# Performance work log

Measured on AMD Instinct MI355X. Metric: run time of the kernel, lower is better.

## Reference

```python
import jax, jax.numpy as jnp
import numpy as np

N = 100000
E = 1600000
IN_DIM, HID, OUT = 128, 64, 32
SLOPE = 0.1


def setup_inputs() -> dict:
    key = jax.random.key(0)
    ks = jax.random.split(key, 8)
    x = jax.random.normal(ks[0], (N, IN_DIM), dtype=jnp.float32)
    edge_index = jax.random.randint(ks[1], (2, E), 0, N, dtype=jnp.int64)
    s1 = 1.0 / np.sqrt(IN_DIM)
    s2 = 1.0 / np.sqrt(HID)
    W_l1 = jax.random.uniform(ks[2], (IN_DIM, HID), jnp.float32, -s1, s1)
    W_r1 = jax.random.uniform(ks[3], (IN_DIM, HID), jnp.float32, -s1, s1)
    b1 = jax.random.uniform(ks[4], (HID,), jnp.float32, -s1, s1)
    W_l2 = jax.random.uniform(ks[5], (HID, OUT), jnp.float32, -s2, s2)
    W_r2 = jax.random.uniform(ks[6], (HID, OUT), jnp.float32, -s2, s2)
    b2 = jax.random.uniform(ks[7], (OUT,), jnp.float32, -s2, s2)
    return {"x": x, "edge_index": edge_index,
            "W_l1": W_l1, "W_r1": W_r1, "b1": b1,
            "W_l2": W_l2, "W_r2": W_r2, "b2": b2}


def _sage_conv(h, src, dst, deg_inv, W_l, W_r, b):
    # mean-aggregate neighbor features: gather from src, scatter-add to dst
    agg = jax.ops.segment_sum(h[src], dst, num_segments=N) * deg_inv  # [N, d]
    return agg @ W_l + h @ W_r + b


def reference(x, edge_index, W_l1, W_r1, b1, W_l2, W_r2, b2):
    src, dst = edge_index[0], edge_index[1]
    deg = jax.ops.segment_sum(jnp.ones((E,), x.dtype), dst, num_segments=N)
    deg_inv = (1.0 / jnp.maximum(deg, 1.0))[:, None]  # [N, 1]
    h = jax.nn.leaky_relu(_sage_conv(x, src, dst, deg_inv, W_l1, W_r1, b1), SLOPE)
    z = jax.nn.leaky_relu(_sage_conv(h, src, dst, deg_inv, W_l2, W_r2, b2), SLOPE)
    return z
```

## Files before the change

### kernel.cpp

```cpp
#include <hip/hip_runtime.h>


constexpr int IN_DIM  = 128;
constexpr int HID     = 64;
constexpr int OUT_DIM = 32;
constexpr float SLOPE = 0.1f;
constexpr int NPB_SHIFT = 8;
constexpr int NBMAX = 512;
constexpr int CHUNK = 4096;
constexpr int SUBCAP = 4096;

typedef unsigned int uint32;
typedef unsigned short ushort16;
typedef unsigned char uchar8;
using floatx2 = __attribute__((ext_vector_type(2))) float;

__device__ inline float blo(uint32 u) { return __uint_as_float(u << 16); }
__device__ inline float bhi(uint32 u) { return __uint_as_float(u & 0xffff0000u); }
__device__ inline ushort16 f2b(float f) {
    uint32 u = __float_as_uint(f);
    u += 0x7fffu + ((u >> 16) & 1u);
    return (ushort16)(u >> 16);
}
__device__ inline uint32 pack2(float lo, float hi) {
    return (uint32)f2b(lo) | ((uint32)f2b(hi) << 16);
}
__device__ inline float lrelu(float v) { return (v > 0.f) ? v : SLOPE * v; }
__device__ inline void addup(float* acc, uint4 u) {
    acc[0] += blo(u.x); acc[1] += bhi(u.x);
    acc[2] += blo(u.y); acc[3] += bhi(u.y);
    acc[4] += blo(u.z); acc[5] += bhi(u.z);
    acc[6] += blo(u.w); acc[7] += bhi(u.w);
}
__device__ inline uchar8 f2fp8(float f) {
    uint32 r = (uint32)__builtin_amdgcn_cvt_pk_fp8_f32(f, f, 0, false);
    return (uchar8)(r & 0xffu);
}
__device__ inline void addp4(float* acc, uint32 w) {
    floatx2 a = __builtin_amdgcn_cvt_pk_f32_fp8((int)w, false);
    floatx2 b = __builtin_amdgcn_cvt_pk_f32_fp8((int)w, true);
    acc[0] += a[0]; acc[1] += a[1]; acc[2] += b[0]; acc[3] += b[1];
}
__device__ inline void addq8(float* acc, uint2 u) {
    addp4(acc + 0, u.x); addp4(acc + 4, u.y);
}

__global__ __launch_bounds__(256) void prep_kernel(
    const float* __restrict__ Wl1, const float* __restrict__ Wr1,
    const float* __restrict__ Wl2, const float* __restrict__ Wr2,
    ushort16* __restrict__ Wb1, ushort16* __restrict__ Wb2,
    int* __restrict__ bhist, int* __restrict__ done) {
    const int gid = blockIdx.x * 256 + threadIdx.x;
    if (gid < NBMAX) bhist[gid] = 0;
    if (gid == NBMAX) *done = 0;
    for (int i = gid; i < 128 * 128; i += gridDim.x * 256) {
        int c = i >> 7, k = i & 127;
        Wb1[i] = f2b((c < HID) ? Wl1[k * HID + c] : Wr1[k * HID + (c - HID)]);
    }
    for (int i = gid; i < 64 * 64; i += gridDim.x * 256) {
        int c = i >> 6, k = i & 63;
        Wb2[i] = f2b((c < OUT_DIM) ? Wl2[k * OUT_DIM + c]
                                   : Wr2[k * OUT_DIM + (c - OUT_DIM)]);
    }
}

__global__ __launch_bounds__(256) void hist_scan_kernel(
    const int* __restrict__ dst, int* __restrict__ bhist,
    int* __restrict__ pbase, int* __restrict__ bcur,
    int* __restrict__ done, int E, int NB) {
    __shared__ int bh[NBMAX];
    __shared__ int s2[256];
    __shared__ int flag;
    const int tid = threadIdx.x;
    for (int i = tid; i < NBMAX; i += 256) bh[i] = 0;
    __syncthreads();
    for (int e = blockIdx.x * 256 + tid; e < E; e += gridDim.x * 256)
        atomicAdd(&bh[dst[e] >> NPB_SHIFT], 1);
    __syncthreads();
    for (int b = tid; b < NBMAX; b += 256)
        if (bh[b]) atomicAdd(&bhist[b], bh[b]);
    __threadfence();
    if (tid == 0) flag = (atomicAdd(done, 1) == (int)gridDim.x - 1) ? 1 : 0;
    __syncthreads();
    if (!flag) return;
    __threadfence();
    int v0 = atomicAdd(&bhist[2 * tid], 0);
    int v1 = atomicAdd(&bhist[2 * tid + 1], 0);
    int p0 = (v0 + 15) & ~15, p1 = (v1 + 15) & ~15;
    s2[tid] = p0 + p1; __syncthreads();
    for (int off = 1; off < 256; off <<= 1) {
        int b = (tid >= off) ? s2[tid - off] : 0;
        __syncthreads();
        s2[tid] += b;
        __syncthreads();
    }
    int base = s2[tid] - (p0 + p1);
    pbase[2 * tid]     = base;      bcur[2 * tid]     = base;
    pbase[2 * tid + 1] = base + p0; bcur[2 * tid + 1] = base + p0;
}

__global__ __launch_bounds__(256) void gemm1_part_kernel(
    const float* __restrict__ x, const ushort16* __restrict__ Wb1,
    const float* __restrict__ b1,
    const int* __restrict__ src, const int* __restrict__ dst,
    int* __restrict__ bcur, uint32* __restrict__ pairs,
    ushort16* __restrict__ xl, float* __restrict__ xr,
    int N, int E, int NB, int npart) {
    using frag = __attribute__((ext_vector_type(8))) short;
    using f32x4 = __attribute__((ext_vector_type(4))) float;
    constexpr int LDA = IN_DIM + 8;
    __shared__ union {
        struct {
            int hist[NBMAX], loff[NBMAX], cur[NBMAX], gbase[NBMAX];
            int s[256];
            uint32 stage[CHUNK];
        } p;
        ushort16 Ash[64][LDA];
    } sm;
    const int tid = threadIdx.x;
    if (blockIdx.x < npart) {
        const int e0  = blockIdx.x * CHUNK;
        const int cnt = min(CHUNK, E - e0);
        for (int i = tid; i < NBMAX; i += 256) sm.p.hist[i] = 0;
        __syncthreads();
        int sreg[16], dreg[16];
#pragma unroll
        for (int k = 0; k < 16; ++k) {
            int i = tid + k * 256;
            if (i < cnt) {
                sreg[k] = src[e0 + i];
                dreg[k] = dst[e0 + i];
                atomicAdd(&sm.p.hist[dreg[k] >> NPB_SHIFT], 1);
            }
        }
        __syncthreads();
        int a0 = sm.p.hist[2 * tid], a1 = sm.p.hist[2 * tid + 1];
        sm.p.s[tid] = a0 + a1; __syncthreads();
        for (int off = 1; off < 256; off <<= 1) {
            int t = (tid >= off) ? sm.p.s[tid - off] : 0;
            __syncthreads();
            sm.p.s[tid] += t;
            __syncthreads();
        }
        int ex = sm.p.s[tid] - (a0 + a1);
        sm.p.loff[2 * tid] = ex;      sm.p.loff[2 * tid + 1] = ex + a0;
        sm.p.cur[2 * tid]  = ex;      sm.p.cur[2 * tid + 1]  = ex + a0;
        __syncthreads();
#pragma unroll
        for (int k = 0; k < 16; ++k) {
            int i = tid + k * 256;
            if (i < cnt) {
                int b = dreg[k] >> NPB_SHIFT;
                int pos = atomicAdd(&sm.p.cur[b], 1);
                sm.p.stage[pos] = (uint32)sreg[k] | ((uint32)(dreg[k] & 255) << 24);
            }
        }
        __syncthreads();
        for (int b = tid; b < NB; b += 256) {
            int cb = sm.p.hist[b];
            if (cb) sm.p.gbase[b] = atomicAdd(&bcur[b], cb);
        }
        __syncthreads();
        for (int i = tid; i < cnt; i += 256) {
            int lo = 0, hi = NB - 1;
            while (lo < hi) {
                int mid = (lo + hi + 1) >> 1;
                if (sm.p.loff[mid] <= i) lo = mid; else hi = mid - 1;
            }
            pairs[sm.p.gbase[lo] + (i - sm.p.loff[lo])] = sm.p.stage[i];
        }
        return;
    }
    const int n0 = (blockIdx.x - npart) * 64;
    {
        const int lc = (tid & 31) * 4;
        for (int row = tid >> 5; row < 64; row += 8) {
            int node = n0 + row;
            float4 xv = (node < N)
                ? *reinterpret_cast<const float4*>(&x[(long)node * IN_DIM + lc])
                : float4{0.f, 0.f, 0.f, 0.f};
            ushort16 pk[4] = {f2b(xv.x), f2b(xv.y), f2b(xv.z), f2b(xv.w)};
            *reinterpret_cast<ushort2*>(&sm.Ash[row][lc])     = ushort2{pk[0], pk[1]};
            *reinterpret_cast<ushort2*>(&sm.Ash[row][lc + 2]) = ushort2{pk[2], pk[3]};
        }
    }
    __syncthreads();
    const int lane = tid & 63;
    const int m0   = (tid >> 6) * 16;
    const int mlo  = lane & 15;
    const int qk   = lane >> 4;
    frag Af[4];
#pragma unroll
    for (int kc = 0; kc < 4; ++kc)
        Af[kc] = *reinterpret_cast<const frag*>(&sm.Ash[m0 + mlo][kc * 32 + qk * 8]);
#pragma unroll
    for (int ct = 0; ct < 8; ++ct) {
        f32x4 acc = {0.f, 0.f, 0.f, 0.f};
#pragma unroll
        for (int kc = 0; kc < 4; ++kc) {
            frag Bf = *reinterpret_cast<const frag*>(
                &Wb1[(ct * 16 + mlo) * 128 + kc * 32 + qk * 8]);
            acc = __builtin_amdgcn_mfma_f32_16x16x32_bf16(Af[kc], Bf, acc, 0, 0, 0);
        }
        const int col = ct * 16 + mlo;
#pragma unroll
        for (int r = 0; r < 4; ++r) {
            int node = n0 + m0 + qk * 4 + r;
            if (node < N) {
                if (col < HID) xl[(long)node * HID + col] = f2b(acc[r]);
                else           xr[(long)node * HID + (col - HID)] = acc[r] + b1[col - HID];
            }
        }
    }
}

__global__ __launch_bounds__(512) void agg1_gemm2_kernel(
    const uint32* __restrict__ pairs, const int* __restrict__ bhist,
    const int* __restrict__ pbase,
    const uint4* __restrict__ xlq, const float* __restrict__ xr,
    const ushort16* __restrict__ Wb2, const float* __restrict__ b2,
    uint32* __restrict__ srcs, int* __restrict__ rowptr, int* __restrict__ degA,
    uchar8* __restrict__ hl8, float* __restrict__ hr, int N) {
    using frag = __attribute__((ext_vector_type(8))) short;
    using f32x4 = __attribute__((ext_vector_type(4))) float;
    constexpr int LDH = HID + 8;
    __shared__ int hist[256], loff[256], cur[128];
    __shared__ int lsrc[SUBCAP];
    __shared__ ushort16 hsh[128][LDH];
    const int tid  = threadIdx.x;
    const int bkt  = blockIdx.x >> 1;
    const int half = blockIdx.x & 1;
    const int n0   = bkt << NPB_SHIFT;
    const int base = pbase[bkt];
    const int sz   = bhist[bkt];
    if (tid < 256) hist[tid] = 0;
    __syncthreads();
    for (int i = tid; i < sz; i += 512)
        atomicAdd(&hist[pairs[base + i] >> 24], 1);
    __syncthreads();
    int v = (tid < 256) ? hist[tid] : 0;
    if (tid < 256) loff[tid] = v;
    __syncthreads();
    for (int off = 1; off < 256; off <<= 1) {
        int t = (tid >= off && tid < 256) ? loff[tid - off] : 0;
        __syncthreads();
        if (tid < 256) loff[tid] += t;
        __syncthreads();
    }
    if (tid < 256) loff[tid] -= v;
    __syncthreads();
    if (half == 0 && tid < 256 && n0 + tid < N) {
        rowptr[n0 + tid] = base + loff[tid];
        degA[n0 + tid]   = hist[tid];
    }
    const int hbase = loff[half << 7];
    const int hcnt  = (half ? sz : loff[128]) - hbase;
    if (tid < 128) cur[tid] = loff[(half << 7) + tid] - hbase;
    __syncthreads();
    for (int i = tid; i < sz; i += 512) {
        uint32 u = pairs[base + i];
        int dl = u >> 24;
        if ((dl >> 7) == half) {
            int pos = atomicAdd(&cur[dl & 127], 1);
            lsrc[pos] = (int)(u & 0xFFFFFFu);
        }
    }
    __syncthreads();
    for (int i = tid; i < hcnt; i += 512)
        srcs[base + hbase + i] = (uint32)lsrc[i];
    const int lane = tid & 63;
    const int wid  = tid >> 6;
    const int li   = lane & 7;
#pragma unroll
    for (int pass = 0; pass < 2; ++pass) {
        const int nll = pass * 64 + wid * 8 + (lane >> 3);
        const int nl  = (half << 7) + nll;
        const int n   = n0 + nl;
        if (n >= N) continue;
        const int lo0 = loff[nl] - hbase;
        const int d   = hist[nl];
        float acc[8] = {};
        int j = 0;
        while (j + 16 <= d) {
            int i0[8], i1[8];
#pragma unroll
            for (int t = 0; t < 8; ++t) i0[t] = lsrc[lo0 + j + t];
#pragma unroll
            for (int t = 0; t < 8; ++t) i1[t] = lsrc[lo0 + j + 8 + t];
            uint4 u0[8], u1[8];
#pragma unroll
            for (int t = 0; t < 8; ++t) u0[t] = xlq[(long)i0[t] * 8 + li];
#pragma unroll
            for (int t = 0; t < 8; ++t) u1[t] = xlq[(long)i1[t] * 8 + li];
#pragma unroll
            for (int t = 0; t < 8; ++t) { addup(acc, u0[t]); addup(acc, u1[t]); }
            j += 16;
        }
        if (j + 8 <= d) {
            int i0[8];
#pragma unroll
            for (int t = 0; t < 8; ++t) i0[t] = lsrc[lo0 + j + t];
            uint4 u0[8];
#pragma unroll
            for (int t = 0; t < 8; ++t) u0[t] = xlq[(long)i0[t] * 8 + li];
#pragma unroll
            for (int t = 0; t < 8; ++t) addup(acc, u0[t]);
            j += 8;
        }
        for (; j < d; ++j) {
            uint4 u = xlq[(long)lsrc[lo0 + j] * 8 + li];
            addup(acc, u);
        }
        const float dinv = (d > 0) ? (1.f / (float)d) : 1.f;
        float4 xrA = *reinterpret_cast<const float4*>(&xr[(long)n * HID + 8 * li]);
        float4 xrB = *reinterpret_cast<const float4*>(&xr[(long)n * HID + 8 * li + 4]);
        float h[8];
        h[0] = fmaf(acc[0], dinv, xrA.x); h[1] = fmaf(acc[1], dinv, xrA.y);
        h[2] = fmaf(acc[2], dinv, xrA.z); h[3] = fmaf(acc[3], dinv, xrA.w);
        h[4] = fmaf(acc[4], dinv, xrB.x); h[5] = fmaf(acc[5], dinv, xrB.y);
        h[6] = fmaf(acc[6], dinv, xrB.z); h[7] = fmaf(acc[7], dinv, xrB.w);
#pragma unroll
        for (int t = 0; t < 8; ++t) h[t] = lrelu(h[t]);
        uint4 pk;
        pk.x = pack2(h[0], h[1]); pk.y = pack2(h[2], h[3]);
        pk.z = pack2(h[4], h[5]); pk.w = pack2(h[6], h[7]);
        *reinterpret_cast<uint4*>(&hsh[nll][li * 8]) = pk;
    }
    __syncthreads();
    const int m0  = wid * 16;
    const int mlo = lane & 15;
    const int qk  = lane >> 4;
    frag Af[2];
#pragma unroll
    for (int kc = 0; kc < 2; ++kc)
        Af[kc] = *reinterpret_cast<const frag*>(&hsh[m0 + mlo][kc * 32 + qk * 8]);
#pragma unroll
    for (int ct = 0; ct < 4; ++ct) {
        f32x4 acc = {0.f, 0.f, 0.f, 0.f};
#pragma unroll
        for (int kc = 0; kc < 2; ++kc) {
            frag Bf = *reinterpret_cast<const frag*>(
                &Wb2[(ct * 16 + mlo) * 64 + kc * 32 + qk * 8]);
            acc = __builtin_amdgcn_mfma_f32_16x16x32_bf16(Af[kc], Bf, acc, 0, 0, 0);
        }
        const int col = ct * 16 + mlo;
#pragma unroll
        for (int r = 0; r < 4; ++r) {
            int node = n0 + (half << 7) + m0 + qk * 4 + r;
            if (node < N) {
                if (col < OUT_DIM) hl8[(long)node * OUT_DIM + col] = f2fp8(acc[r]);
                else hr[(long)node * OUT_DIM + (col - OUT_DIM)] = acc[r] + b2[col - OUT_DIM];
            }
        }
    }
}

__global__ __launch_bounds__(256) void agg2_final_kernel(
    const int* __restrict__ rowptr, const int* __restrict__ degA,
    const uint32* __restrict__ srcs,
    const uint2* __restrict__ hlq, const float* __restrict__ hr,
    float* __restrict__ z, int N) {
    const int lane  = threadIdx.x & 63;
    const int li    = lane & 3;
    const int gbase = lane & 60;
    const int wave  = (blockIdx.x << 2) + (threadIdx.x >> 6);
    const int n     = wave * 16 + (lane >> 2);
    if (n >= N) return;
    const int rp = rowptr[n];
    const int d  = degA[n];
    float acc[8] = {};
    int j = 0;
    while (j + 16 <= d) {
        int sA = (int)srcs[rp + j + li];
        int sB = (int)srcs[rp + j + 4 + li];
        int sC = (int)srcs[rp + j + 8 + li];
        int sD = (int)srcs[rp + j + 12 + li];
        uint2 u[16];
#pragma unroll
        for (int t = 0; t < 4; ++t) u[t]      = hlq[(long)__shfl(sA, gbase + t) * 4 + li];
#pragma unroll
        for (int t = 0; t < 4; ++t) u[4 + t]  = hlq[(long)__shfl(sB, gbase + t) * 4 + li];
#pragma unroll
        for (int t = 0; t < 4; ++t) u[8 + t]  = hlq[(long)__shfl(sC, gbase + t) * 4 + li];
#pragma unroll
        for (int t = 0; t < 4; ++t) u[12 + t] = hlq[(long)__shfl(sD, gbase + t) * 4 + li];
#pragma unroll
        for (int t = 0; t < 16; ++t) addq8(acc, u[t]);
        j += 16;
    }
    while (j + 4 <= d) {
        int sA = (int)srcs[rp + j + li];
        uint2 u[4];
#pragma unroll
        for (int t = 0; t < 4; ++t) u[t] = hlq[(long)__shfl(sA, gbase + t) * 4 + li];
#pragma unroll
        for (int t = 0; t < 4; ++t) addq8(acc, u[t]);
        j += 4;
    }
    int r = d - j;
    if (r > 0) {
        int sA = (int)srcs[rp + j + ((li < r) ? li : 0)];
#pragma unroll
        for (int t = 0; t < 3; ++t) {
            if (t < r) {
                uint2 u = hlq[(long)__shfl(sA, gbase + t) * 4 + li];
                addq8(acc, u);
            }
        }
    }
    const float dinv = (d > 0) ? (1.f / (float)d) : 1.f;
    float4 hA = *reinterpret_cast<const float4*>(&hr[(long)n * OUT_DIM + 8 * li]);
    float4 hB = *reinterpret_cast<const float4*>(&hr[(long)n * OUT_DIM + 8 * li + 4]);
    float4 vA, vB;
    vA.x = lrelu(fmaf(acc[0], dinv, hA.x)); vA.y = lrelu(fmaf(acc[1], dinv, hA.y));
    vA.z = lrelu(fmaf(acc[2], dinv, hA.z)); vA.w = lrelu(fmaf(acc[3], dinv, hA.w));
    vB.x = lrelu(fmaf(acc[4], dinv, hB.x)); vB.y = lrelu(fmaf(acc[5], dinv, hB.y));
    vB.z = lrelu(fmaf(acc[6], dinv, hB.z)); vB.w = lrelu(fmaf(acc[7], dinv, hB.w));
    *reinterpret_cast<float4*>(&z[(long)n * OUT_DIM + 8 * li]) = vA;
    *reinterpret_cast<float4*>(&z[(long)n * OUT_DIM + 8 * li + 4]) = vB;
}

extern "C" void kernel_launch(void* const* d_in, const int* in_sizes, int n_in,
                              void* d_out, int out_size, void* d_ws, size_t ws_size,
                              hipStream_t stream) {
    const float* x   = (const float*)d_in[0];
    const int*   ei  = (const int*)d_in[1];
    const float* Wl1 = (const float*)d_in[2];
    const float* Wr1 = (const float*)d_in[3];
    const float* b1  = (const float*)d_in[4];
    const float* Wl2 = (const float*)d_in[5];
    const float* Wr2 = (const float*)d_in[6];
    const float* b2  = (const float*)d_in[7];

    const int N = in_sizes[0] / IN_DIM;
    const int E = in_sizes[1] / 2;
    const int* src = ei;
    const int* dst = ei + E;
    const int NB = (N + 255) >> NPB_SHIFT;

    char* p = (char*)d_ws;
    int* bhist    = (int*)p;           p += sizeof(int) * NBMAX;
    int* done     = (int*)p;           p += sizeof(int) * 4;
    int* pbase    = (int*)p;           p += sizeof(int) * NBMAX;
    int* bcur     = (int*)p;           p += sizeof(int) * NBMAX;
    int* rowptr   = (int*)p;           p += sizeof(int) * (N + 4);
    int* degA     = (int*)p;           p += sizeof(int) * (N + 4);
    uint32* pairs = (uint32*)p;        p += sizeof(uint32) * ((size_t)E + 16 * NBMAX);
    uint32* srcs  = (uint32*)p;        p += sizeof(uint32) * ((size_t)E + 16 * NBMAX);
    ushort16* Wb1 = (ushort16*)p;      p += sizeof(ushort16) * 128 * 128;
    ushort16* Wb2 = (ushort16*)p;      p += sizeof(ushort16) * 64 * 64;
    ushort16* xl  = (ushort16*)p;      p += sizeof(ushort16) * (size_t)N * HID;
    float* xr     = (float*)p;         p += sizeof(float) * (size_t)N * HID;
    uchar8* hl8   = (uchar8*)p;        p += sizeof(uchar8) * ((size_t)N * OUT_DIM + 64);
    float* hr     = (float*)p;         p += sizeof(float) * (size_t)N * OUT_DIM;

    const int ngemm = (N + 63) / 64;
    const int npart = (E + CHUNK - 1) / CHUNK;
    prep_kernel<<<32, 256, 0, stream>>>(Wl1, Wr1, Wl2, Wr2, Wb1, Wb2, bhist, done);
    hist_scan_kernel<<<256, 256, 0, stream>>>(dst, bhist, pbase, bcur, done, E, NB);
    gemm1_part_kernel<<<npart + ngemm, 256, 0, stream>>>(
        x, Wb1, b1, src, dst, bcur, pairs, xl, xr, N, E, NB, npart);
    agg1_gemm2_kernel<<<NB * 2, 512, 0, stream>>>(pairs, bhist, pbase,
                                                  (const uint4*)xl, xr, Wb2, b2,
                                                  srcs, rowptr, degA, hl8, hr, N);
    agg2_final_kernel<<<(N + 63) / 64, 256, 0, stream>>>(rowptr, degA, srcs,
                                                         (const uint2*)hl8, hr,
                                                         (float*)d_out, N);
}
```

Measured before the change: 278.7 us.

## Store root-term intermediates in bf16 and stage GEMM outputs through LDS

```diff
diff --git a/kernel.cpp b/kernel.cpp
--- a/kernel.cpp
+++ b/kernel.cpp
@@ -104,7 +104,7 @@
     const float* __restrict__ b1,
     const int* __restrict__ src, const int* __restrict__ dst,
     int* __restrict__ bcur, uint32* __restrict__ pairs,
-    ushort16* __restrict__ xl, float* __restrict__ xr,
+    ushort16* __restrict__ xl, ushort16* __restrict__ xr,
     int N, int E, int NB, int npart) {
     using frag = __attribute__((ext_vector_type(8))) short;
     using f32x4 = __attribute__((ext_vector_type(4))) float;
@@ -116,6 +116,7 @@
             uint32 stage[CHUNK];
         } p;
         ushort16 Ash[64][LDA];
+        ushort16 xst[2][64][64];
     } sm;
     const int tid = threadIdx.x;
     if (blockIdx.x < npart) {
@@ -193,6 +194,7 @@
 #pragma unroll
     for (int kc = 0; kc < 4; ++kc)
         Af[kc] = *reinterpret_cast<const frag*>(&sm.Ash[m0 + mlo][kc * 32 + qk * 8]);
+    __syncthreads();
 #pragma unroll
     for (int ct = 0; ct < 8; ++ct) {
         f32x4 acc = {0.f, 0.f, 0.f, 0.f};
@@ -205,11 +207,20 @@
         const int col = ct * 16 + mlo;
 #pragma unroll
         for (int r = 0; r < 4; ++r) {
-            int node = n0 + m0 + qk * 4 + r;
-            if (node < N) {
-                if (col < HID) xl[(long)node * HID + col] = f2b(acc[r]);
-                else           xr[(long)node * HID + (col - HID)] = acc[r] + b1[col - HID];
-            }
+            int row = m0 + qk * 4 + r;
+            if (col < HID) sm.xst[0][row][col] = f2b(acc[r]);
+            else           sm.xst[1][row][col - HID] = f2b(acc[r] + b1[col - HID]);
+        }
+    }
+    __syncthreads();
+    for (int idx = tid; idx < 64 * 8; idx += 256) {
+        int row = idx >> 3, ch = idx & 7;
+        int node = n0 + row;
+        if (node < N) {
+            reinterpret_cast<uint4*>(xl)[(long)node * 8 + ch] =
+                reinterpret_cast<const uint4*>(&sm.xst[0][0][0])[idx];
+            reinterpret_cast<uint4*>(xr)[(long)node * 8 + ch] =
+                reinterpret_cast<const uint4*>(&sm.xst[1][0][0])[idx];
         }
     }
 }
@@ -217,10 +228,10 @@
 __global__ __launch_bounds__(512) void agg1_gemm2_kernel(
     const uint32* __restrict__ pairs, const int* __restrict__ bhist,
     const int* __restrict__ pbase,
-    const uint4* __restrict__ xlq, const float* __restrict__ xr,
+    const uint4* __restrict__ xlq, const uint4* __restrict__ xrq,
     const ushort16* __restrict__ Wb2, const float* __restrict__ b2,
     uint32* __restrict__ srcs, int* __restrict__ rowptr, int* __restrict__ degA,
-    uchar8* __restrict__ hl8, float* __restrict__ hr, int N) {
+    uchar8* __restrict__ hl8, ushort16* __restrict__ hr, int N) {
     using frag = __attribute__((ext_vector_type(8))) short;
     using f32x4 = __attribute__((ext_vector_type(4))) float;
     constexpr int LDH = HID + 8;
@@ -312,13 +323,12 @@
             addup(acc, u);
         }
         const float dinv = (d > 0) ? (1.f / (float)d) : 1.f;
-        float4 xrA = *reinterpret_cast<const float4*>(&xr[(long)n * HID + 8 * li]);
-        float4 xrB = *reinterpret_cast<const float4*>(&xr[(long)n * HID + 8 * li + 4]);
+        uint4 xv = xrq[(long)n * 8 + li];
         float h[8];
-        h[0] = fmaf(acc[0], dinv, xrA.x); h[1] = fmaf(acc[1], dinv, xrA.y);
-        h[2] = fmaf(acc[2], dinv, xrA.z); h[3] = fmaf(acc[3], dinv, xrA.w);
-        h[4] = fmaf(acc[4], dinv, xrB.x); h[5] = fmaf(acc[5], dinv, xrB.y);
-        h[6] = fmaf(acc[6], dinv, xrB.z); h[7] = fmaf(acc[7], dinv, xrB.w);
+        h[0] = fmaf(acc[0], dinv, blo(xv.x)); h[1] = fmaf(acc[1], dinv, bhi(xv.x));
+        h[2] = fmaf(acc[2], dinv, blo(xv.y)); h[3] = fmaf(acc[3], dinv, bhi(xv.y));
+        h[4] = fmaf(acc[4], dinv, blo(xv.z)); h[5] = fmaf(acc[5], dinv, bhi(xv.z));
+        h[6] = fmaf(acc[6], dinv, blo(xv.w)); h[7] = fmaf(acc[7], dinv, bhi(xv.w));
 #pragma unroll
         for (int t = 0; t < 8; ++t) h[t] = lrelu(h[t]);
         uint4 pk;
@@ -327,6 +337,8 @@
         *reinterpret_cast<uint4*>(&hsh[nll][li * 8]) = pk;
     }
     __syncthreads();
+    unsigned char* hl_st = reinterpret_cast<unsigned char*>(lsrc);
+    ushort16* hr_st = reinterpret_cast<ushort16*>(lsrc + 1024);
     const int m0  = wid * 16;
     const int mlo = lane & 15;
     const int qk  = lane >> 4;
@@ -346,19 +358,32 @@
         const int col = ct * 16 + mlo;
 #pragma unroll
         for (int r = 0; r < 4; ++r) {
-            int node = n0 + (half << 7) + m0 + qk * 4 + r;
-            if (node < N) {
-                if (col < OUT_DIM) hl8[(long)node * OUT_DIM + col] = f2fp8(acc[r]);
-                else hr[(long)node * OUT_DIM + (col - OUT_DIM)] = acc[r] + b2[col - OUT_DIM];
-            }
-        }
+            int row = m0 + qk * 4 + r;
+            if (col < OUT_DIM) hl_st[row * 32 + col] = f2fp8(acc[r]);
+            else hr_st[row * 32 + (col - OUT_DIM)] = f2b(acc[r] + b2[col - OUT_DIM]);
+        }
+    }
+    __syncthreads();
+    for (int idx = tid; idx < 128 * 2; idx += 512) {
+        int row = idx >> 1, ch = idx & 1;
+        int node = n0 + (half << 7) + row;
+        if (node < N)
+            reinterpret_cast<uint4*>(hl8)[(long)node * 2 + ch] =
+                reinterpret_cast<const uint4*>(hl_st)[idx];
+    }
+    for (int idx = tid; idx < 128 * 4; idx += 512) {
+        int row = idx >> 2, ch = idx & 3;
+        int node = n0 + (half << 7) + row;
+        if (node < N)
+            reinterpret_cast<uint4*>(hr)[(long)node * 4 + ch] =
+                reinterpret_cast<const uint4*>(hr_st)[idx];
     }
 }
 
 __global__ __launch_bounds__(256) void agg2_final_kernel(
     const int* __restrict__ rowptr, const int* __restrict__ degA,
     const uint32* __restrict__ srcs,
-    const uint2* __restrict__ hlq, const float* __restrict__ hr,
+    const uint2* __restrict__ hlq, const uint4* __restrict__ hrq,
     float* __restrict__ z, int N) {
     const int lane  = threadIdx.x & 63;
     const int li    = lane & 3;
@@ -409,13 +434,12 @@
         }
     }
     const float dinv = (d > 0) ? (1.f / (float)d) : 1.f;
-    float4 hA = *reinterpret_cast<const float4*>(&hr[(long)n * OUT_DIM + 8 * li]);
-    float4 hB = *reinterpret_cast<const float4*>(&hr[(long)n * OUT_DIM + 8 * li + 4]);
+    uint4 hv = hrq[(long)n * 4 + li];
     float4 vA, vB;
-    vA.x = lrelu(fmaf(acc[0], dinv, hA.x)); vA.y = lrelu(fmaf(acc[1], dinv, hA.y));
-    vA.z = lrelu(fmaf(acc[2], dinv, hA.z)); vA.w = lrelu(fmaf(acc[3], dinv, hA.w));
-    vB.x = lrelu(fmaf(acc[4], dinv, hB.x)); vB.y = lrelu(fmaf(acc[5], dinv, hB.y));
-    vB.z = lrelu(fmaf(acc[6], dinv, hB.z)); vB.w = lrelu(fmaf(acc[7], dinv, hB.w));
+    vA.x = lrelu(fmaf(acc[0], dinv, blo(hv.x))); vA.y = lrelu(fmaf(acc[1], dinv, bhi(hv.x)));
+    vA.z = lrelu(fmaf(acc[2], dinv, blo(hv.y))); vA.w = lrelu(fmaf(acc[3], dinv, bhi(hv.y)));
+    vB.x = lrelu(fmaf(acc[4], dinv, blo(hv.z))); vB.y = lrelu(fmaf(acc[5], dinv, bhi(hv.z)));
+    vB.z = lrelu(fmaf(acc[6], dinv, blo(hv.w))); vB.w = lrelu(fmaf(acc[7], dinv, bhi(hv.w)));
     *reinterpret_cast<float4*>(&z[(long)n * OUT_DIM + 8 * li]) = vA;
     *reinterpret_cast<float4*>(&z[(long)n * OUT_DIM + 8 * li + 4]) = vB;
 }
@@ -450,9 +474,9 @@
     ushort16* Wb1 = (ushort16*)p;      p += sizeof(ushort16) * 128 * 128;
     ushort16* Wb2 = (ushort16*)p;      p += sizeof(ushort16) * 64 * 64;
     ushort16* xl  = (ushort16*)p;      p += sizeof(ushort16) * (size_t)N * HID;
-    float* xr     = (float*)p;         p += sizeof(float) * (size_t)N * HID;
+    ushort16* xr  = (ushort16*)p;      p += sizeof(ushort16) * ((size_t)N * HID + 8);
     uchar8* hl8   = (uchar8*)p;        p += sizeof(uchar8) * ((size_t)N * OUT_DIM + 64);
-    float* hr     = (float*)p;         p += sizeof(float) * (size_t)N * OUT_DIM;
+    ushort16* hr  = (ushort16*)p;      p += sizeof(ushort16) * ((size_t)N * OUT_DIM + 8);
 
     const int ngemm = (N + 63) / 64;
     const int npart = (E + CHUNK - 1) / CHUNK;
@@ -461,9 +485,11 @@
     gemm1_part_kernel<<<npart + ngemm, 256, 0, stream>>>(
         x, Wb1, b1, src, dst, bcur, pairs, xl, xr, N, E, NB, npart);
     agg1_gemm2_kernel<<<NB * 2, 512, 0, stream>>>(pairs, bhist, pbase,
-                                                  (const uint4*)xl, xr, Wb2, b2,
+                                                  (const uint4*)xl, (const uint4*)xr,
+                                                  Wb2, b2,
                                                   srcs, rowptr, degA, hl8, hr, N);
     agg2_final_kernel<<<(N + 63) / 64, 256, 0, stream>>>(rowptr, degA, srcs,
-                                                         (const uint2*)hl8, hr,
+                                                         (const uint2*)hl8,
+                                                         (const uint4*)hr,
                                                          (float*)d_out, N);
 }
```

New measurement: 259.8 us. -6.8%, faster.
